# Kernel tuning notes

Hardware: AMD Instinct MI355X
Metric: run time of the kernel (lower is better)

## Reference

```python
import jax, jax.numpy as jnp
import numpy as np

N_NODES = 50000
N_EDGES = 800000
N_GRAPHS = 64
IN_C = 32
OUT_C = 10
BN_EPS = 1e-5


def _glorot(key, shape):
    lim = float(np.sqrt(6.0 / (shape[0] + shape[1])))
    return jax.random.uniform(key, shape, jnp.float32, -lim, lim)


def gcn_conv(x, W, b, src, dst, n):
    # PyG GCNConv: x' = D^-1/2 (A + I) D^-1/2 (x W) + b, deg over dst incl. self-loop
    h = x @ W                                              # [N, C_out]
    deg = jax.ops.segment_sum(jnp.ones(src.shape[0], h.dtype), dst,
                              num_segments=n) + 1.0        # +1 self-loop
    dinv = jnp.where(deg > 0, 1.0 / jnp.sqrt(deg), 0.0)    # [N]
    norm = dinv[src] * dinv[dst]                           # [E]
    agg = jax.ops.segment_sum(h[src] * norm[:, None], dst, num_segments=n)
    agg = agg + h * (dinv * dinv)[:, None]                 # self-loop messages
    return agg + b


def bn_eval(x, gamma, beta):
    # BatchNorm1d in eval mode with freshly-initialized running stats (mean=0, var=1)
    return x * (gamma / jnp.sqrt(1.0 + BN_EPS)) + beta


def setup_inputs() -> dict:
    key = jax.random.key(0)
    ks = jax.random.split(key, 12)
    x = jax.random.normal(ks[0], (N_NODES, IN_C), jnp.float32)
    edge_src = jax.random.randint(ks[1], (N_EDGES,), 0, N_NODES)
    edge_dst = jax.random.randint(ks[2], (N_EDGES,), 0, N_NODES)
    batch = jnp.sort(jax.random.randint(ks[3], (N_NODES,), 0, N_GRAPHS))
    c1, c2 = IN_C * 2, IN_C * 4
    return {
        "x": x, "edge_src": edge_src, "edge_dst": edge_dst, "batch": batch,
        "W1": _glorot(ks[4], (IN_C, c1)), "b1": jnp.zeros((c1,), jnp.float32),
        "W2": _glorot(ks[5], (c1, c2)),   "b2": jnp.zeros((c2,), jnp.float32),
        "W3": _glorot(ks[6], (c2, 32)),   "b3": jnp.zeros((32,), jnp.float32),
        "g3": jnp.ones((32,), jnp.float32), "beta3": jnp.zeros((32,), jnp.float32),
        "W4": _glorot(ks[7], (32, 64)),   "b4": jnp.zeros((64,), jnp.float32),
        "g4": jnp.ones((64,), jnp.float32), "beta4": jnp.zeros((64,), jnp.float32),
        "W5": _glorot(ks[8], (64, OUT_C)), "b5": jnp.zeros((OUT_C,), jnp.float32),
    }


def reference(x, edge_src, edge_dst, batch,
              W1, b1, W2, b2, W3, b3, g3, beta3,
              W4, b4, g4, beta4, W5, b5):
    h = jax.nn.relu(gcn_conv(x, W1, b1, edge_src, edge_dst, N_NODES))
    h = jax.nn.relu(gcn_conv(h, W2, b2, edge_src, edge_dst, N_NODES))
    pooled = jax.ops.segment_max(h, batch, num_segments=N_GRAPHS)   # [B, 4*IN_C]
    z = bn_eval(jax.nn.relu(pooled @ W3 + b3), g3, beta3)
    z = bn_eval(jax.nn.relu(z @ W4 + b4), g4, beta4)
    logits = z @ W5 + b5
    return jax.nn.log_softmax(logits, axis=1)
```

## Files before the change

kernel.cpp:

```cpp
#include <hip/hip_runtime.h>
#include <hip/hip_bf16.h>

#define N_NODES_C 50000
#define N_EDGES_C 800000
#define N_GRAPHS_C 64
#define NPAD 50176
#define NBKT 392
#define BKT_CAP 32
#define P1_BLOCKS 256
#define P1_THREADS 512
#define BKT_TOTAL_CAP 2432
#define SC 64

__device__ __forceinline__ ushort f2bf(float f) {
    unsigned u = __float_as_uint(f);
    return (ushort)((u + 0x7FFFu + ((u >> 16) & 1u)) >> 16);
}
__device__ __forceinline__ void bf8_add(float* acc, uint4 v) {
    acc[0] += __uint_as_float(v.x << 16);
    acc[1] += __uint_as_float(v.x & 0xFFFF0000u);
    acc[2] += __uint_as_float(v.y << 16);
    acc[3] += __uint_as_float(v.y & 0xFFFF0000u);
    acc[4] += __uint_as_float(v.z << 16);
    acc[5] += __uint_as_float(v.z & 0xFFFF0000u);
    acc[6] += __uint_as_float(v.w << 16);
    acc[7] += __uint_as_float(v.w & 0xFFFF0000u);
}

__global__ __launch_bounds__(P1_THREADS) void k_bucket(
        const int* __restrict__ src, const int* __restrict__ dst,
        int* __restrict__ cnt1, unsigned* __restrict__ ent,
        float4* __restrict__ pooled4, int nE) {
    __shared__ int cur[NBKT];
    for (int i = threadIdx.x; i < NBKT; i += P1_THREADS) cur[i] = 0;
    {
        int idx = blockIdx.x * P1_THREADS + threadIdx.x;
        if (idx < 2048) pooled4[idx] = make_float4(0.f, 0.f, 0.f, 0.f);
    }
    __syncthreads();
    const int per = (nE + P1_BLOCKS - 1) / P1_BLOCKS;
    const int lo = blockIdx.x * per;
    const int hi = min(nE, lo + per);
    unsigned* entB = ent + (size_t)blockIdx.x * NBKT * BKT_CAP;
    for (int e = lo + threadIdx.x; e < hi; e += P1_THREADS) {
        int d = dst[e];
        int b = d >> 7;
        int p = atomicAdd(&cur[b], 1);
        if (p < BKT_CAP)
            entB[b * BKT_CAP + p] = (unsigned)src[e] | ((unsigned)(d & 127) << 16);
    }
    __syncthreads();
    for (int i = threadIdx.x; i < NBKT; i += P1_THREADS)
        cnt1[i * P1_BLOCKS + blockIdx.x] = min(cur[i], BKT_CAP);
}

__global__ __launch_bounds__(256) void k_build(
        const int* __restrict__ cnt1, const unsigned* __restrict__ ent,
        const float* __restrict__ x,
        int* __restrict__ cntT, float* __restrict__ dinv,
        ushort* __restrict__ slots, ushort* __restrict__ xs, int n) {
    __shared__ unsigned stage[BKT_TOTAL_CAP];
    __shared__ ushort sout[128 * SC];
    __shared__ int scnt[128], scur[128];
    __shared__ float sdinv[128];
    __shared__ int stotal;
    const int bkt = blockIdx.x;
    const int tid = threadIdx.x;
    if (tid == 0) stotal = 0;
    if (tid < 128) { scnt[tid] = 0; scur[tid] = 0; }
    __syncthreads();
    const int c = cnt1[bkt * P1_BLOCKS + tid];
    int base = atomicAdd(&stotal, c);
    const unsigned* cell = ent + ((size_t)tid * NBKT + bkt) * BKT_CAP;
    for (int j = 0; j < c; ++j) {
        unsigned e = cell[j];
        if (base + j < BKT_TOTAL_CAP) stage[base + j] = e;
        atomicAdd(&scnt[e >> 16], 1);
    }
    __syncthreads();
    const int total = min(stotal, BKT_TOTAL_CAP);
    for (int i = tid; i < total; i += 256) {
        unsigned e = stage[i];
        int node = e >> 16;
        int p = atomicAdd(&scur[node], 1);
        if (p < SC) sout[node * SC + p] = (ushort)(e & 0xFFFF);
    }
    __syncthreads();
    float4* gs = (float4*)(slots + (size_t)bkt * 128 * SC);
    const float4* ls = (const float4*)sout;
    for (int i = tid; i < 128 * SC * 2 / 16; i += 256) gs[i] = ls[i];
    if (tid < 128) {
        int node = bkt * 128 + tid;
        int deg = scnt[tid];
        float dv = rsqrtf((float)deg + 1.0f);
        sdinv[tid] = dv;
        cntT[node] = min(deg, SC);
        dinv[node] = dv;
    }
    __syncthreads();
    const float4* __restrict__ x4 = (const float4*)x;
    uint4* __restrict__ xs4 = (uint4*)xs;
    for (int i = tid; i < 128 * 4; i += 256) {
        int row = i >> 2, q = i & 3;
        int node = bkt * 128 + row;
        if (node < n) {
            float dv = sdinv[row];
            float4 a = x4[(size_t)node * 8 + q * 2];
            float4 b = x4[(size_t)node * 8 + q * 2 + 1];
            uint4 o;
            o.x = (unsigned)f2bf(a.x * dv) | ((unsigned)f2bf(a.y * dv) << 16);
            o.y = (unsigned)f2bf(a.z * dv) | ((unsigned)f2bf(a.w * dv) << 16);
            o.z = (unsigned)f2bf(b.x * dv) | ((unsigned)f2bf(b.y * dv) << 16);
            o.w = (unsigned)f2bf(b.z * dv) | ((unsigned)f2bf(b.w * dv) << 16);
            xs4[(size_t)node * 4 + q] = o;
        }
    }
}

template<int C>
__global__ __launch_bounds__(256) void k_gather(
        const ushort* __restrict__ Y, const float* __restrict__ dinv,
        const int* __restrict__ cntT, const ushort* __restrict__ slots,
        float* __restrict__ OUT, int n) {
    constexpr int LPN = C / 8;
    constexpr int NPB = 256 / LPN;
    const int node = blockIdx.x * NPB + threadIdx.x / LPN;
    const int lane = threadIdx.x % LPN;
    if (node >= n) return;
    const int m = cntT[node];
    const ushort* __restrict__ sl = &slots[(size_t)node * SC];
    const uint4* __restrict__ Y4 = (const uint4*)Y;
    float acc[8] = {0.f, 0.f, 0.f, 0.f, 0.f, 0.f, 0.f, 0.f};
    bf8_add(acc, Y4[(size_t)node * LPN + lane]);
    int j = 0;
    for (; j + 4 <= m; j += 4) {
        ushort4 s4 = *(const ushort4*)&sl[j];
        uint4 a = Y4[(size_t)s4.x * LPN + lane];
        uint4 b = Y4[(size_t)s4.y * LPN + lane];
        uint4 c = Y4[(size_t)s4.z * LPN + lane];
        uint4 d = Y4[(size_t)s4.w * LPN + lane];
        bf8_add(acc, a); bf8_add(acc, b); bf8_add(acc, c); bf8_add(acc, d);
    }
    for (; j < m; ++j) bf8_add(acc, Y4[(size_t)sl[j] * LPN + lane]);
    const float dd = dinv[node];
    float4* O4 = (float4*)OUT;
    O4[(size_t)node * (C / 4) + lane * 2] =
        make_float4(acc[0] * dd, acc[1] * dd, acc[2] * dd, acc[3] * dd);
    O4[(size_t)node * (C / 4) + lane * 2 + 1] =
        make_float4(acc[4] * dd, acc[5] * dd, acc[6] * dd, acc[7] * dd);
}

template<int CIN, int COUT, int ROWS, bool POOL, bool SCALE>
__global__ __launch_bounds__(256) void k_mm(
        const float* __restrict__ X, const float* __restrict__ W,
        const float* __restrict__ bias, const float* __restrict__ dinv,
        void* __restrict__ H, const int* __restrict__ batch,
        unsigned* __restrict__ P, int n) {
    constexpr int TN = 4;
    constexpr int COLG = COUT / TN;
    constexpr int ROWG = 256 / COLG;
    constexpr int TM = ROWS / ROWG;
    __shared__ float sW[CIN * COUT];
    __shared__ float sx[ROWS * CIN];
    __shared__ int sBatch[ROWS];
    __shared__ float sDinv[ROWS];

    const int tid = threadIdx.x;
    for (int i = tid; i < CIN * COUT / 4; i += 256)
        ((float4*)sW)[i] = ((const float4*)W)[i];

    const int cg = tid % COLG;
    const int rg = tid / COLG;
    const float4 bv = ((const float4*)bias)[cg];

    const int base = blockIdx.x * ROWS;
    __syncthreads();
    for (int i = tid; i < ROWS * CIN / 4; i += 256) {
        int rr = i / (CIN / 4), k4 = i % (CIN / 4);
        int grow = base + rr;
        float4 v = make_float4(0.f, 0.f, 0.f, 0.f);
        if (grow < n) v = ((const float4*)X)[(size_t)grow * (CIN / 4) + k4];
        ((float4*)sx)[i] = v;
    }
    if (POOL) {
        for (int i = tid; i < ROWS; i += 256)
            sBatch[i] = (base + i < n) ? batch[base + i] : -1;
    }
    if (SCALE) {
        for (int i = tid; i < ROWS; i += 256)
            sDinv[i] = (base + i < n) ? dinv[base + i] : 0.f;
    }
    __syncthreads();

    float acc[TM][TN];
#pragma unroll
    for (int i = 0; i < TM; ++i)
#pragma unroll
        for (int j = 0; j < TN; ++j) acc[i][j] = 0.f;

    const float* sxrow = &sx[rg * TM * CIN];
#pragma unroll 4
    for (int k = 0; k < CIN; ++k) {
        float4 w = *(const float4*)&sW[k * COUT + cg * TN];
#pragma unroll
        for (int i = 0; i < TM; ++i) {
            float xv = sxrow[i * CIN + k];
            acc[i][0] = fmaf(xv, w.x, acc[i][0]);
            acc[i][1] = fmaf(xv, w.y, acc[i][1]);
            acc[i][2] = fmaf(xv, w.z, acc[i][2]);
            acc[i][3] = fmaf(xv, w.w, acc[i][3]);
        }
    }

    if (!POOL) {
#pragma unroll
        for (int i = 0; i < TM; ++i) {
            int row = base + rg * TM + i;
            if (row >= n) continue;
            float4 v;
            v.x = acc[i][0] + bv.x; v.x = v.x > 0.f ? v.x : 0.f;
            v.y = acc[i][1] + bv.y; v.y = v.y > 0.f ? v.y : 0.f;
            v.z = acc[i][2] + bv.z; v.z = v.z > 0.f ? v.z : 0.f;
            v.w = acc[i][3] + bv.w; v.w = v.w > 0.f ? v.w : 0.f;
            if (SCALE) {
                float sc = sDinv[rg * TM + i];
                v.x *= sc; v.y *= sc; v.z *= sc; v.w *= sc;
                uint2 o;
                o.x = (unsigned)f2bf(v.x) | ((unsigned)f2bf(v.y) << 16);
                o.y = (unsigned)f2bf(v.z) | ((unsigned)f2bf(v.w) << 16);
                ((uint2*)H)[((size_t)row * COUT + cg * TN) / 4] = o;
            } else {
                ((float4*)H)[((size_t)row * COUT + cg * TN) / 4] = v;
            }
        }
    } else {
        static_assert(!POOL || (ROWS == 64 && COUT == 128), "pool path tuned for 64x128");
        float* sPool = sx;
#pragma unroll
        for (int h = 0; h < 2; ++h) {
            __syncthreads();
            if (rg >= h * 4 && rg < (h + 1) * 4) {
                const int rlo = rg * TM - h * 32;
#pragma unroll
                for (int i = 0; i < TM; ++i) {
                    float4 v;
                    v.x = acc[i][0] + bv.x; v.x = v.x > 0.f ? v.x : 0.f;
                    v.y = acc[i][1] + bv.y; v.y = v.y > 0.f ? v.y : 0.f;
                    v.z = acc[i][2] + bv.z; v.z = v.z > 0.f ? v.z : 0.f;
                    v.w = acc[i][3] + bv.w; v.w = v.w > 0.f ? v.w : 0.f;
                    *(float4*)&sPool[(rlo + i) * COUT + cg * TN] = v;
                }
            }
            __syncthreads();
            const int c = tid % COUT;
            const int rblk = tid / COUT;
            int gprev = -1;
            float m = 0.f;
            for (int r = rblk * 16; r < rblk * 16 + 16; ++r) {
                int grow = base + h * 32 + r;
                if (grow >= n) break;
                int g = sBatch[h * 32 + r];
                float v = sPool[r * COUT + c];
                if (g != gprev) {
                    if (gprev >= 0)
                        atomicMax(&P[(size_t)gprev * COUT + c], __float_as_uint(m));
                    gprev = g; m = v;
                } else {
                    m = fmaxf(m, v);
                }
            }
            if (gprev >= 0)
                atomicMax(&P[(size_t)gprev * COUT + c], __float_as_uint(m));
        }
    }
}

__global__ void k_head(const float* __restrict__ P,
                       const float* __restrict__ W3, const float* __restrict__ b3,
                       const float* __restrict__ g3, const float* __restrict__ beta3,
                       const float* __restrict__ W4, const float* __restrict__ b4,
                       const float* __restrict__ g4, const float* __restrict__ beta4,
                       const float* __restrict__ W5, const float* __restrict__ b5,
                       float* __restrict__ out) {
    __shared__ float sP[128];
    __shared__ float sz3[32];
    __shared__ float sz4[64];
    __shared__ float slg[10];
    __shared__ float slse;
    const int g = blockIdx.x, tid = threadIdx.x;
    sP[tid] = P[g * 128 + tid];
    __syncthreads();
    const float bnscale = rsqrtf(1.0f + 1e-5f);

    if (tid < 32) {
        float a = 0.f;
#pragma unroll
        for (int k = 0; k < 128; ++k) a = fmaf(sP[k], W3[k * 32 + tid], a);
        a += b3[tid];
        a = a > 0.f ? a : 0.f;
        sz3[tid] = a * (g3[tid] * bnscale) + beta3[tid];
    }
    __syncthreads();
    if (tid < 64) {
        float a = 0.f;
#pragma unroll
        for (int k = 0; k < 32; ++k) a = fmaf(sz3[k], W4[k * 64 + tid], a);
        a += b4[tid];
        a = a > 0.f ? a : 0.f;
        sz4[tid] = a * (g4[tid] * bnscale) + beta4[tid];
    }
    __syncthreads();
    if (tid < 10) {
        float a = 0.f;
#pragma unroll
        for (int k = 0; k < 64; ++k) a = fmaf(sz4[k], W5[k * 10 + tid], a);
        slg[tid] = a + b5[tid];
    }
    __syncthreads();
    if (tid == 0) {
        float m = -1e30f;
#pragma unroll
        for (int j = 0; j < 10; ++j) m = fmaxf(m, slg[j]);
        float s = 0.f;
#pragma unroll
        for (int j = 0; j < 10; ++j) s += expf(slg[j] - m);
        slse = m + logf(s);
    }
    __syncthreads();
    if (tid < 10) out[g * 10 + tid] = slg[tid] - slse;
}

extern "C" void kernel_launch(void* const* d_in, const int* in_sizes, int n_in,
                              void* d_out, int out_size, void* d_ws, size_t ws_size,
                              hipStream_t stream) {
    const float* x        = (const float*)d_in[0];
    const int*   edge_src = (const int*)d_in[1];
    const int*   edge_dst = (const int*)d_in[2];
    const int*   batch    = (const int*)d_in[3];
    const float* W1 = (const float*)d_in[4];
    const float* b1 = (const float*)d_in[5];
    const float* W2 = (const float*)d_in[6];
    const float* b2 = (const float*)d_in[7];
    const float* W3 = (const float*)d_in[8];
    const float* b3 = (const float*)d_in[9];
    const float* g3 = (const float*)d_in[10];
    const float* beta3 = (const float*)d_in[11];
    const float* W4 = (const float*)d_in[12];
    const float* b4 = (const float*)d_in[13];
    const float* g4 = (const float*)d_in[14];
    const float* beta4 = (const float*)d_in[15];
    const float* W5 = (const float*)d_in[16];
    const float* b5 = (const float*)d_in[17];
    float* out = (float*)d_out;

    const int n  = in_sizes[0] / 32;
    const int nE = in_sizes[1];

    char* wsb = (char*)d_ws;
    int*      cnt1   = (int*)wsb;
    unsigned* ent    = (unsigned*)(cnt1 + NBKT * P1_BLOCKS);
    int*      cntT   = (int*)(ent + (size_t)P1_BLOCKS * NBKT * BKT_CAP);
    float*    dinv   = (float*)(cntT + NPAD);
    ushort*   slots  = (ushort*)(dinv + NPAD);
    ushort*   xs     = slots + (size_t)NPAD * SC;
    float*    buf1   = (float*)(xs + (size_t)NPAD * 32);
    ushort*   h1s    = (ushort*)(buf1 + (size_t)n * 64);
    float*    pooled = (float*)(h1s + (size_t)n * 64);
    float*    aggX   = buf1;
    float*    agg2   = buf1;

    k_bucket<<<P1_BLOCKS, P1_THREADS, 0, stream>>>(edge_src, edge_dst, cnt1, ent,
                                                   (float4*)pooled, nE);
    k_build<<<NBKT, 256, 0, stream>>>(cnt1, ent, x, cntT, dinv, slots, xs, n);

    k_gather<32><<<(n + 63) / 64, 256, 0, stream>>>(xs, dinv, cntT, slots, aggX, n);
    k_mm<32, 64, 128, false, true><<<(n + 127) / 128, 256, 0, stream>>>(
        aggX, W1, b1, dinv, h1s, nullptr, nullptr, n);

    k_gather<64><<<(n + 31) / 32, 256, 0, stream>>>(h1s, dinv, cntT, slots, agg2, n);
    k_mm<64, 128, 64, true, false><<<(n + 63) / 64, 256, 0, stream>>>(
        agg2, W2, b2, nullptr, nullptr, batch, (unsigned*)pooled, n);

    k_head<<<64, 128, 0, stream>>>(pooled, W3, b3, g3, beta3, W4, b4, g4, beta4, W5, b5, out);
}
```

Baseline: 94.14 us.

## Fuse neighbor gather into matmul kernels, keeping aggregates in shared memory

Merges the separate gather and matmul kernels for each GCN layer into one kernel. Each block first aggregates its rows' neighbor features into shared memory, then runs the dense transform and epilogue on them. This removes the fp32 intermediate write and read of the aggregates and two kernel launches. The weight matrix is now read from global memory or cache instead of being staged in shared memory. Blocks are larger per gather phase, which may cut parallelism and latency hiding for the irregular gathers.

```diff
diff --git a/kernel.cpp b/kernel.cpp
--- a/kernel.cpp
+++ b/kernel.cpp
@@ -117,80 +117,66 @@
     }
 }
 
-template<int C>
-__global__ __launch_bounds__(256) void k_gather(
+template<int CIN, int COUT, int ROWS, bool POOL, bool SCALE>
+__global__ __launch_bounds__(256) void k_gmm(
         const ushort* __restrict__ Y, const float* __restrict__ dinv,
         const int* __restrict__ cntT, const ushort* __restrict__ slots,
-        float* __restrict__ OUT, int n) {
-    constexpr int LPN = C / 8;
-    constexpr int NPB = 256 / LPN;
-    const int node = blockIdx.x * NPB + threadIdx.x / LPN;
-    const int lane = threadIdx.x % LPN;
-    if (node >= n) return;
-    const int m = cntT[node];
-    const ushort* __restrict__ sl = &slots[(size_t)node * SC];
-    const uint4* __restrict__ Y4 = (const uint4*)Y;
-    float acc[8] = {0.f, 0.f, 0.f, 0.f, 0.f, 0.f, 0.f, 0.f};
-    bf8_add(acc, Y4[(size_t)node * LPN + lane]);
-    int j = 0;
-    for (; j + 4 <= m; j += 4) {
-        ushort4 s4 = *(const ushort4*)&sl[j];
-        uint4 a = Y4[(size_t)s4.x * LPN + lane];
-        uint4 b = Y4[(size_t)s4.y * LPN + lane];
-        uint4 c = Y4[(size_t)s4.z * LPN + lane];
-        uint4 d = Y4[(size_t)s4.w * LPN + lane];
-        bf8_add(acc, a); bf8_add(acc, b); bf8_add(acc, c); bf8_add(acc, d);
-    }
-    for (; j < m; ++j) bf8_add(acc, Y4[(size_t)sl[j] * LPN + lane]);
-    const float dd = dinv[node];
-    float4* O4 = (float4*)OUT;
-    O4[(size_t)node * (C / 4) + lane * 2] =
-        make_float4(acc[0] * dd, acc[1] * dd, acc[2] * dd, acc[3] * dd);
-    O4[(size_t)node * (C / 4) + lane * 2 + 1] =
-        make_float4(acc[4] * dd, acc[5] * dd, acc[6] * dd, acc[7] * dd);
-}
-
-template<int CIN, int COUT, int ROWS, bool POOL, bool SCALE>
-__global__ __launch_bounds__(256) void k_mm(
-        const float* __restrict__ X, const float* __restrict__ W,
-        const float* __restrict__ bias, const float* __restrict__ dinv,
+        const float* __restrict__ W, const float* __restrict__ bias,
         void* __restrict__ H, const int* __restrict__ batch,
         unsigned* __restrict__ P, int n) {
     constexpr int TN = 4;
     constexpr int COLG = COUT / TN;
     constexpr int ROWG = 256 / COLG;
     constexpr int TM = ROWS / ROWG;
-    __shared__ float sW[CIN * COUT];
-    __shared__ float sx[ROWS * CIN];
+    constexpr int LPN = CIN / 8;
+    constexpr int NPB = 256 / LPN;
+    constexpr int NPASS = ROWS / NPB;
+
+    __shared__ float sAgg[ROWS * CIN];
     __shared__ int sBatch[ROWS];
     __shared__ float sDinv[ROWS];
 
     const int tid = threadIdx.x;
-    for (int i = tid; i < CIN * COUT / 4; i += 256)
-        ((float4*)sW)[i] = ((const float4*)W)[i];
+    const int base = blockIdx.x * ROWS;
+    const uint4* __restrict__ Y4 = (const uint4*)Y;
+
+#pragma unroll
+    for (int ps = 0; ps < NPASS; ++ps) {
+        const int nl = ps * NPB + tid / LPN;
+        const int lane = tid % LPN;
+        const int node = base + nl;
+        if (node < n) {
+            const int m = cntT[node];
+            const ushort* __restrict__ sl = &slots[(size_t)node * SC];
+            float acc[8] = {0.f, 0.f, 0.f, 0.f, 0.f, 0.f, 0.f, 0.f};
+            bf8_add(acc, Y4[(size_t)node * LPN + lane]);
+            int j = 0;
+            for (; j + 4 <= m; j += 4) {
+                ushort4 s4 = *(const ushort4*)&sl[j];
+                uint4 a = Y4[(size_t)s4.x * LPN + lane];
+                uint4 b = Y4[(size_t)s4.y * LPN + lane];
+                uint4 c = Y4[(size_t)s4.z * LPN + lane];
+                uint4 d = Y4[(size_t)s4.w * LPN + lane];
+                bf8_add(acc, a); bf8_add(acc, b); bf8_add(acc, c); bf8_add(acc, d);
+            }
+            for (; j < m; ++j) bf8_add(acc, Y4[(size_t)sl[j] * LPN + lane]);
+            const float dd = dinv[node];
+#pragma unroll
+            for (int q = 0; q < 8; ++q) sAgg[nl * CIN + lane * 8 + q] = acc[q] * dd;
+            if (lane == 0) {
+                if (SCALE) sDinv[nl] = dd;
+                if (POOL) sBatch[nl] = batch[node];
+            }
+        } else if (lane == 0 && POOL) {
+            sBatch[nl] = -1;
+        }
+    }
+    __syncthreads();
 
     const int cg = tid % COLG;
     const int rg = tid / COLG;
     const float4 bv = ((const float4*)bias)[cg];
-
-    const int base = blockIdx.x * ROWS;
-    __syncthreads();
-    for (int i = tid; i < ROWS * CIN / 4; i += 256) {
-        int rr = i / (CIN / 4), k4 = i % (CIN / 4);
-        int grow = base + rr;
-        float4 v = make_float4(0.f, 0.f, 0.f, 0.f);
-        if (grow < n) v = ((const float4*)X)[(size_t)grow * (CIN / 4) + k4];
-        ((float4*)sx)[i] = v;
-    }
-    if (POOL) {
-        for (int i = tid; i < ROWS; i += 256)
-            sBatch[i] = (base + i < n) ? batch[base + i] : -1;
-    }
-    if (SCALE) {
-        for (int i = tid; i < ROWS; i += 256)
-            sDinv[i] = (base + i < n) ? dinv[base + i] : 0.f;
-    }
-    __syncthreads();
+    const float4* __restrict__ Wv = (const float4*)W;
 
     float acc[TM][TN];
 #pragma unroll
@@ -198,10 +184,10 @@
 #pragma unroll
         for (int j = 0; j < TN; ++j) acc[i][j] = 0.f;
 
-    const float* sxrow = &sx[rg * TM * CIN];
+    const float* sxrow = &sAgg[rg * TM * CIN];
 #pragma unroll 4
     for (int k = 0; k < CIN; ++k) {
-        float4 w = *(const float4*)&sW[k * COUT + cg * TN];
+        float4 w = Wv[k * COLG + cg];
 #pragma unroll
         for (int i = 0; i < TM; ++i) {
             float xv = sxrow[i * CIN + k];
@@ -234,8 +220,9 @@
             }
         }
     } else {
-        static_assert(!POOL || (ROWS == 64 && COUT == 128), "pool path tuned for 64x128");
-        float* sPool = sx;
+        static_assert(!POOL || (ROWS == 64 && COUT == 128 && CIN == 64),
+                      "pool path tuned for 64x64->128");
+        float* sPool = sAgg;
 #pragma unroll
         for (int h = 0; h < 2; ++h) {
             __syncthreads();
@@ -363,23 +350,18 @@
     float*    dinv   = (float*)(cntT + NPAD);
     ushort*   slots  = (ushort*)(dinv + NPAD);
     ushort*   xs     = slots + (size_t)NPAD * SC;
-    float*    buf1   = (float*)(xs + (size_t)NPAD * 32);
-    ushort*   h1s    = (ushort*)(buf1 + (size_t)n * 64);
-    float*    pooled = (float*)(h1s + (size_t)n * 64);
-    float*    aggX   = buf1;
-    float*    agg2   = buf1;
+    ushort*   h1s    = xs + (size_t)NPAD * 32;
+    float*    pooled = (float*)(h1s + (size_t)NPAD * 64);
 
     k_bucket<<<P1_BLOCKS, P1_THREADS, 0, stream>>>(edge_src, edge_dst, cnt1, ent,
                                                    (float4*)pooled, nE);
     k_build<<<NBKT, 256, 0, stream>>>(cnt1, ent, x, cntT, dinv, slots, xs, n);
 
-    k_gather<32><<<(n + 63) / 64, 256, 0, stream>>>(xs, dinv, cntT, slots, aggX, n);
-    k_mm<32, 64, 128, false, true><<<(n + 127) / 128, 256, 0, stream>>>(
-        aggX, W1, b1, dinv, h1s, nullptr, nullptr, n);
-
-    k_gather<64><<<(n + 31) / 32, 256, 0, stream>>>(h1s, dinv, cntT, slots, agg2, n);
-    k_mm<64, 128, 64, true, false><<<(n + 63) / 64, 256, 0, stream>>>(
-        agg2, W2, b2, nullptr, nullptr, batch, (unsigned*)pooled, n);
+    k_gmm<32, 64, 128, false, true><<<(n + 127) / 128, 256, 0, stream>>>(
+        xs, dinv, cntT, slots, W1, b1, h1s, nullptr, nullptr, n);
+
+    k_gmm<64, 128, 64, true, false><<<(n + 63) / 64, 256, 0, stream>>>(
+        h1s, dinv, cntT, slots, W2, b2, nullptr, batch, (unsigned*)pooled, n);
 
     k_head<<<64, 128, 0, stream>>>(pooled, W3, b3, g3, beta3, W4, b4, g4, beta4, W5, b5, out);
 }
```

New measurement: 85.52 us. -9.2%, faster.
